# Kernel optimization log

Measured on AMD Instinct MI355X. Metric: run time of the kernel, lower is better.

The kernel has to match this reference:

```python
import jax, jax.numpy as jnp
import numpy as np

N = 100_000   # total nodes across all subgraphs in batch
E = 1_600_000 # edges (avg degree 16)
B = 1_000     # number of subgraphs
D = 128       # in_dim = out_dim
SZ = N // B   # nodes per subgraph


def setup_inputs() -> dict:
    key = jax.random.key(0)
    ks = jax.random.split(key, 8)
    feat = jax.random.normal(ks[0], (N, D), dtype=jnp.float32)
    edge_src = jax.random.randint(ks[1], (E,), 0, N, dtype=jnp.int32)
    edge_dst = jax.random.randint(ks[2], (E,), 0, N, dtype=jnp.int32)
    # pre-normalized edge weights (is_normed=True path)
    edge_w = jax.random.uniform(ks[3], (E,), dtype=jnp.float32)
    s = 1.0 / np.sqrt(D)
    W1 = jax.random.normal(ks[4], (D, D), dtype=jnp.float32) * s
    W2 = jax.random.normal(ks[5], (D, D), dtype=jnp.float32) * s
    Wp = jax.random.normal(ks[6], (D, D), dtype=jnp.float32) * s
    b1 = jnp.zeros((D,), jnp.float32)
    b2 = jnp.zeros((D,), jnp.float32)
    bp = jnp.zeros((D,), jnp.float32)
    # contiguous equal-size subgraphs; target = first node of each subgraph
    seg_ids = jnp.repeat(jnp.arange(B, dtype=jnp.int32), SZ)
    target = jnp.arange(B, dtype=jnp.int32) * SZ
    size_subg = jnp.full((B,), float(SZ), jnp.float32)
    return dict(feat=feat, edge_w=edge_w, W1=W1, b1=b1, W2=W2, b2=b2,
                Wp=Wp, bp=bp, size_subg=size_subg,
                edge_src=edge_src, edge_dst=edge_dst,
                seg_ids=seg_ids, target=target)


def _gcn_layer(x, src, dst, w, W, b):
    # sparse A_hat @ x : gather src features, weight, scatter-add into dst
    msg = x[src] * w[:, None]                       # [E, D]
    agg = jax.ops.segment_sum(msg, dst, num_segments=N)  # [N, D]
    return jax.nn.relu(agg @ W + b)


def reference(feat, edge_w, W1, b1, W2, b2, Wp, bp, size_subg,
              edge_src, edge_dst, seg_ids, target):
    # two stacked GCN layers (self.structure = [structure1, structure2])
    h1 = _gcn_layer(feat, edge_src, edge_dst, edge_w, W1, b1)
    h2 = _gcn_layer(h1, edge_src, edge_dst, edge_w, W2, b2)
    # ResPool: residual-sum over layer outputs, mean pool per subgraph,
    # add target-node embedding (residual), then linear + relu
    h = h1 + h2                                              # [N, D]
    pooled = jax.ops.segment_sum(h, seg_ids, num_segments=B)
    pooled = pooled / size_subg[:, None] + h[target]         # [B, D]
    emb = jax.nn.relu(pooled @ Wp + bp)
    # F.normalize(p=2, dim=1), eps=1e-12
    norm = jnp.sqrt(jnp.sum(emb * emb, axis=1, keepdims=True))
    emb = emb / jnp.maximum(norm, 1e-12)
    return emb  # EnsembleDummy just returns the single branch
```

## Files before the change

### kernel.cpp

```cpp
#include <hip/hip_runtime.h>

#define DD 128
#define CHUNK 4096
#define BSH 8
#define MAXBK 512
#define CAP 6144

typedef _Float16 half8 __attribute__((ext_vector_type(8)));
typedef _Float16 half4v __attribute__((ext_vector_type(4)));
typedef float floatx4 __attribute__((ext_vector_type(4)));
typedef float floatx2 __attribute__((ext_vector_type(2)));

__global__ __launch_bounds__(256) void k_prep(const float* __restrict__ W1,
                                              _Float16* __restrict__ W1t,
                                              const float* __restrict__ W2,
                                              _Float16* __restrict__ W2t) {
    int idx = blockIdx.x * 256 + threadIdx.x;
    const float* W = (idx < DD * DD) ? W1 : W2;
    _Float16* Wt = (idx < DD * DD) ? W1t : W2t;
    int id = idx & (DD * DD - 1);
    int n = id >> 7, k = id & 127;
    Wt[n * DD + k] = (_Float16)W[k * DD + n];
}

__global__ __launch_bounds__(512) void k_p1g1(const int* __restrict__ src,
                                              const int* __restrict__ dst,
                                              const float* __restrict__ w,
                                              int* __restrict__ gcur,
                                              int2* __restrict__ out, int E, int NB,
                                              int p1Blocks,
                                              const float* __restrict__ A,
                                              const _Float16* __restrict__ Wt,
                                              unsigned char* __restrict__ Y, int nrows) {
    if (blockIdx.x < p1Blocks) {
        __shared__ int2 stg[CHUNK];
        __shared__ unsigned short bok[CHUNK];
        __shared__ int lhist[MAXBK];
        __shared__ int loff[MAXBK];
        __shared__ int lbase[MAXBK];
        __shared__ int lcur[MAXBK];
        int tid = threadIdx.x;
        lhist[tid] = 0;
        __syncthreads();

        int beg = blockIdx.x * CHUNK;
        int end = min(beg + CHUNK, E);
        for (int k = beg + tid; k < end; k += 512)
            atomicAdd(&lhist[dst[k] >> BSH], 1);
        __syncthreads();
        if (tid < 64) {
            int base = tid * 8, v[8], s = 0;
            #pragma unroll
            for (int j = 0; j < 8; ++j) { v[j] = lhist[base + j]; s += v[j]; }
            int scn = s;
            #pragma unroll
            for (int off = 1; off < 64; off <<= 1) {
                int t = __shfl_up(scn, off, 64);
                if (tid >= off) scn += t;
            }
            int ex = scn - s;
            #pragma unroll
            for (int j = 0; j < 8; ++j) { loff[base + j] = ex; lcur[base + j] = ex; ex += v[j]; }
        }
        __syncthreads();
        if (tid < NB) {
            int c = lhist[tid];
            if (c) lbase[tid] = tid * CAP + atomicAdd(&gcur[tid], c);
        }
        __syncthreads();
        for (int k = beg + tid; k < end; k += 512) {
            int d = dst[k];
            int b = d >> BSH;
            int p = atomicAdd(&lcur[b], 1);
            stg[p] = make_int2(src[k] | ((d & ((1 << BSH) - 1)) << 17),
                               __float_as_int(w[k]));
            bok[p] = (unsigned short)b;
        }
        __syncthreads();
        int total = end - beg;
        for (int j = tid; j < total; j += 512) {
            int b = bok[j];
            out[lbase[b] + (j - loff[b])] = stg[j];
        }
    } else {
        int gblk = blockIdx.x - p1Blocks;
        int wave = threadIdx.x >> 6;
        int lane = threadIdx.x & 63;
        int row0 = gblk * 256 + wave * 32;
        int m = lane & 15;
        int q = lane >> 4;
        int r0 = min(row0 + m, nrows - 1);
        int r1 = min(row0 + 16 + m, nrows - 1);

        floatx4 acc[2][8];
        #pragma unroll
        for (int t = 0; t < 2; ++t)
            #pragma unroll
            for (int c = 0; c < 8; ++c)
                acc[t][c] = (floatx4){0.f, 0.f, 0.f, 0.f};

        #pragma unroll
        for (int ks = 0; ks < 4; ++ks) {
            int kbase = ks * 32 + q * 8;
            float4 x0 = *reinterpret_cast<const float4*>(A + (size_t)r0 * DD + kbase);
            float4 x1 = *reinterpret_cast<const float4*>(A + (size_t)r0 * DD + kbase + 4);
            float4 y0 = *reinterpret_cast<const float4*>(A + (size_t)r1 * DD + kbase);
            float4 y1 = *reinterpret_cast<const float4*>(A + (size_t)r1 * DD + kbase + 4);
            half8 a0, a1;
            a0[0]=(_Float16)x0.x; a0[1]=(_Float16)x0.y; a0[2]=(_Float16)x0.z; a0[3]=(_Float16)x0.w;
            a0[4]=(_Float16)x1.x; a0[5]=(_Float16)x1.y; a0[6]=(_Float16)x1.z; a0[7]=(_Float16)x1.w;
            a1[0]=(_Float16)y0.x; a1[1]=(_Float16)y0.y; a1[2]=(_Float16)y0.z; a1[3]=(_Float16)y0.w;
            a1[4]=(_Float16)y1.x; a1[5]=(_Float16)y1.y; a1[6]=(_Float16)y1.z; a1[7]=(_Float16)y1.w;
            #pragma unroll
            for (int c = 0; c < 8; ++c) {
                half8 b = *reinterpret_cast<const half8*>(Wt + (size_t)(c * 16 + m) * DD + kbase);
                acc[0][c] = __builtin_amdgcn_mfma_f32_16x16x32_f16(b, a0, acc[0][c], 0, 0, 0);
                acc[1][c] = __builtin_amdgcn_mfma_f32_16x16x32_f16(b, a1, acc[1][c], 0, 0, 0);
            }
        }

        #pragma unroll
        for (int t = 0; t < 2; ++t) {
            int row = row0 + t * 16 + m;
            if (row >= nrows) continue;
            size_t rb = (size_t)row * DD;
            #pragma unroll
            for (int c = 0; c < 8; ++c) {
                int col = c * 16 + q * 4;
                int u = 0;
                u = __builtin_amdgcn_cvt_pk_fp8_f32(acc[t][c][0], acc[t][c][1], u, false);
                u = __builtin_amdgcn_cvt_pk_fp8_f32(acc[t][c][2], acc[t][c][3], u, true);
                *reinterpret_cast<unsigned int*>(&Y[rb + col]) = (unsigned int)u;
            }
        }
    }
}

__global__ __launch_bounds__(512) void k_pass2(const int2* __restrict__ bkt,
                                               const int* __restrict__ gcur,
                                               int2* __restrict__ rows,
                                               int2* __restrict__ edges, int N) {
    __shared__ int lhist[1 << BSH];
    __shared__ int loff[1 << BSH];
    __shared__ int lcur[1 << BSH];
    int tid = threadIdx.x;
    int b = blockIdx.x;
    int base = b * CAP;
    int nrec = gcur[b];
    int d0 = b << BSH;

    if (tid < (1 << BSH)) lhist[tid] = 0;
    __syncthreads();
    for (int i = tid; i < nrec; i += 512)
        atomicAdd(&lhist[(unsigned)bkt[base + i].x >> 17], 1);
    __syncthreads();
    if (tid < 64) {
        int bs = tid * 4, vv[4], s = 0;
        #pragma unroll
        for (int j = 0; j < 4; ++j) { vv[j] = lhist[bs + j]; s += vv[j]; }
        int scn = s;
        #pragma unroll
        for (int off = 1; off < 64; off <<= 1) {
            int t = __shfl_up(scn, off, 64);
            if (tid >= off) scn += t;
        }
        int ex = scn - s;
        #pragma unroll
        for (int j = 0; j < 4; ++j) {
            loff[bs + j] = ex; lcur[bs + j] = ex; ex += vv[j];
        }
    }
    __syncthreads();
    if (tid < (1 << BSH)) {
        int d = d0 + tid;
        if (d < N)
            rows[d] = make_int2(base + loff[tid], base + loff[tid] + lhist[tid]);
    }
    for (int i = tid; i < nrec; i += 512) {
        int2 r = bkt[base + i];
        int dl = (unsigned)r.x >> 17;
        int p = base + atomicAdd(&lcur[dl], 1);
        edges[p] = make_int2(r.x & 0x1FFFF, r.y);
    }
}

__global__ __launch_bounds__(256) void k_gemm_f16A(const _Float16* __restrict__ A,
                                                   const _Float16* __restrict__ Wt,
                                                   unsigned char* __restrict__ Y,
                                                   int nrows) {
    int wave = threadIdx.x >> 6;
    int lane = threadIdx.x & 63;
    int row0 = blockIdx.x * 128 + wave * 32;
    int m = lane & 15;
    int q = lane >> 4;

    floatx4 acc[2][8];
    #pragma unroll
    for (int t = 0; t < 2; ++t)
        #pragma unroll
        for (int c = 0; c < 8; ++c)
            acc[t][c] = (floatx4){0.f, 0.f, 0.f, 0.f};

    #pragma unroll
    for (int ks = 0; ks < 4; ++ks) {
        int kbase = ks * 32 + q * 8;
        half8 a0 = *reinterpret_cast<const half8*>(A + (size_t)(row0 + m) * DD + kbase);
        half8 a1 = *reinterpret_cast<const half8*>(A + (size_t)(row0 + 16 + m) * DD + kbase);
        #pragma unroll
        for (int c = 0; c < 8; ++c) {
            half8 b = *reinterpret_cast<const half8*>(Wt + (size_t)(c * 16 + m) * DD + kbase);
            acc[0][c] = __builtin_amdgcn_mfma_f32_16x16x32_f16(b, a0, acc[0][c], 0, 0, 0);
            acc[1][c] = __builtin_amdgcn_mfma_f32_16x16x32_f16(b, a1, acc[1][c], 0, 0, 0);
        }
    }

    #pragma unroll
    for (int t = 0; t < 2; ++t) {
        int row = row0 + t * 16 + m;
        if (row >= nrows) continue;
        size_t rb = (size_t)row * DD;
        #pragma unroll
        for (int c = 0; c < 8; ++c) {
            int col = c * 16 + q * 4;
            int u = 0;
            u = __builtin_amdgcn_cvt_pk_fp8_f32(acc[t][c][0], acc[t][c][1], u, false);
            u = __builtin_amdgcn_cvt_pk_fp8_f32(acc[t][c][2], acc[t][c][3], u, true);
            *reinterpret_cast<unsigned int*>(&Y[rb + col]) = (unsigned int)u;
        }
    }
}

__global__ __launch_bounds__(256) void k_agg_eplg(const unsigned char* __restrict__ x,
                                                  const int2* __restrict__ rows,
                                                  const int2* __restrict__ edges,
                                                  const float* __restrict__ bias,
                                                  const _Float16* __restrict__ resid,
                                                  _Float16* __restrict__ out, int N) {
    int gwave = (blockIdx.x * blockDim.x + threadIdx.x) >> 6;
    int lane = threadIdx.x & 63;
    int half = lane >> 5;
    int hl = lane & 31;
    int wid = gwave * 2 + half;
    if (wid >= N) return;
    int g = hl >> 3;
    int sl = hl & 7;
    int2 rr = rows[wid];
    int beg = rr.x, end = rr.y;
    float acc[16];
    #pragma unroll
    for (int j = 0; j < 16; ++j) acc[j] = 0.f;

    int i = beg;
    for (; i + 16 <= end; i += 16) {
        int2 e[4];
        #pragma unroll
        for (int u = 0; u < 4; ++u) e[u] = edges[i + u * 4 + g];
        uint4 v[4];
        #pragma unroll
        for (int u = 0; u < 4; ++u)
            v[u] = *reinterpret_cast<const uint4*>(x + (size_t)e[u].x * DD + sl * 16);
        #pragma unroll
        for (int u = 0; u < 4; ++u) {
            float wv = __int_as_float(e[u].y);
            floatx2 f0 = __builtin_amdgcn_cvt_pk_f32_fp8((int)v[u].x, false);
            floatx2 f1 = __builtin_amdgcn_cvt_pk_f32_fp8((int)v[u].x, true);
            floatx2 f2 = __builtin_amdgcn_cvt_pk_f32_fp8((int)v[u].y, false);
            floatx2 f3 = __builtin_amdgcn_cvt_pk_f32_fp8((int)v[u].y, true);
            floatx2 f4 = __builtin_amdgcn_cvt_pk_f32_fp8((int)v[u].z, false);
            floatx2 f5 = __builtin_amdgcn_cvt_pk_f32_fp8((int)v[u].z, true);
            floatx2 f6 = __builtin_amdgcn_cvt_pk_f32_fp8((int)v[u].w, false);
            floatx2 f7 = __builtin_amdgcn_cvt_pk_f32_fp8((int)v[u].w, true);
            acc[0]  = fmaf(f0[0], wv, acc[0]);  acc[1]  = fmaf(f0[1], wv, acc[1]);
            acc[2]  = fmaf(f1[0], wv, acc[2]);  acc[3]  = fmaf(f1[1], wv, acc[3]);
            acc[4]  = fmaf(f2[0], wv, acc[4]);  acc[5]  = fmaf(f2[1], wv, acc[5]);
            acc[6]  = fmaf(f3[0], wv, acc[6]);  acc[7]  = fmaf(f3[1], wv, acc[7]);
            acc[8]  = fmaf(f4[0], wv, acc[8]);  acc[9]  = fmaf(f4[1], wv, acc[9]);
            acc[10] = fmaf(f5[0], wv, acc[10]); acc[11] = fmaf(f5[1], wv, acc[11]);
            acc[12] = fmaf(f6[0], wv, acc[12]); acc[13] = fmaf(f6[1], wv, acc[13]);
            acc[14] = fmaf(f7[0], wv, acc[14]); acc[15] = fmaf(f7[1], wv, acc[15]);
        }
    }
    if (i < end) {
        int2 e[4];
        int ok[4];
        #pragma unroll
        for (int u = 0; u < 4; ++u) {
            int idx = i + u * 4 + g;
            ok[u] = idx < end;
            e[u] = edges[min(idx, end - 1)];
        }
        uint4 v[4];
        #pragma unroll
        for (int u = 0; u < 4; ++u)
            v[u] = *reinterpret_cast<const uint4*>(x + (size_t)e[u].x * DD + sl * 16);
        #pragma unroll
        for (int u = 0; u < 4; ++u) {
            float wv = ok[u] ? __int_as_float(e[u].y) : 0.f;
            floatx2 f0 = __builtin_amdgcn_cvt_pk_f32_fp8((int)v[u].x, false);
            floatx2 f1 = __builtin_amdgcn_cvt_pk_f32_fp8((int)v[u].x, true);
            floatx2 f2 = __builtin_amdgcn_cvt_pk_f32_fp8((int)v[u].y, false);
            floatx2 f3 = __builtin_amdgcn_cvt_pk_f32_fp8((int)v[u].y, true);
            floatx2 f4 = __builtin_amdgcn_cvt_pk_f32_fp8((int)v[u].z, false);
            floatx2 f5 = __builtin_amdgcn_cvt_pk_f32_fp8((int)v[u].z, true);
            floatx2 f6 = __builtin_amdgcn_cvt_pk_f32_fp8((int)v[u].w, false);
            floatx2 f7 = __builtin_amdgcn_cvt_pk_f32_fp8((int)v[u].w, true);
            acc[0]  = fmaf(f0[0], wv, acc[0]);  acc[1]  = fmaf(f0[1], wv, acc[1]);
            acc[2]  = fmaf(f1[0], wv, acc[2]);  acc[3]  = fmaf(f1[1], wv, acc[3]);
            acc[4]  = fmaf(f2[0], wv, acc[4]);  acc[5]  = fmaf(f2[1], wv, acc[5]);
            acc[6]  = fmaf(f3[0], wv, acc[6]);  acc[7]  = fmaf(f3[1], wv, acc[7]);
            acc[8]  = fmaf(f4[0], wv, acc[8]);  acc[9]  = fmaf(f4[1], wv, acc[9]);
            acc[10] = fmaf(f5[0], wv, acc[10]); acc[11] = fmaf(f5[1], wv, acc[11]);
            acc[12] = fmaf(f6[0], wv, acc[12]); acc[13] = fmaf(f6[1], wv, acc[13]);
            acc[14] = fmaf(f7[0], wv, acc[14]); acc[15] = fmaf(f7[1], wv, acc[15]);
        }
    }
    #pragma unroll
    for (int j = 0; j < 16; ++j) {
        acc[j] += __shfl_xor(acc[j], 8, 64);
        acc[j] += __shfl_xor(acc[j], 16, 64);
    }
    if (g == 0) {
        size_t rb = (size_t)wid * DD + sl * 16;
        float bb[16];
        #pragma unroll
        for (int q = 0; q < 4; ++q) {
            float4 b4 = *reinterpret_cast<const float4*>(&bias[sl * 16 + q * 4]);
            bb[q * 4 + 0] = b4.x; bb[q * 4 + 1] = b4.y;
            bb[q * 4 + 2] = b4.z; bb[q * 4 + 3] = b4.w;
        }
        half8 o0, o1;
        if (resid) {
            half8 r0 = *reinterpret_cast<const half8*>(&resid[rb]);
            half8 r1 = *reinterpret_cast<const half8*>(&resid[rb + 8]);
            #pragma unroll
            for (int j = 0; j < 8; ++j) {
                float v = acc[j] + bb[j];
                v = v > 0.f ? v : 0.f;
                o0[j] = (_Float16)(v + (float)r0[j]);
            }
            #pragma unroll
            for (int j = 0; j < 8; ++j) {
                float v = acc[8 + j] + bb[8 + j];
                v = v > 0.f ? v : 0.f;
                o1[j] = (_Float16)(v + (float)r1[j]);
            }
        } else {
            #pragma unroll
            for (int j = 0; j < 8; ++j) {
                float v = acc[j] + bb[j];
                o0[j] = (_Float16)(v > 0.f ? v : 0.f);
            }
            #pragma unroll
            for (int j = 0; j < 8; ++j) {
                float v = acc[8 + j] + bb[8 + j];
                o1[j] = (_Float16)(v > 0.f ? v : 0.f);
            }
        }
        *reinterpret_cast<half8*>(&out[rb]) = o0;
        *reinterpret_cast<half8*>(&out[rb + 8]) = o1;
    }
}

__global__ __launch_bounds__(256) void k_pool_final(const _Float16* __restrict__ h,
                                                    const int* __restrict__ target,
                                                    const float* __restrict__ size_subg,
                                                    const float* __restrict__ Wp,
                                                    const float* __restrict__ bp,
                                                    float* __restrict__ out, int SZ) {
    __shared__ float part[16][DD];
    __shared__ float p[DD];
    __shared__ float wsum[2];
    int b = blockIdx.x;
    int t = threadIdx.x;
    int c = t & 15;
    int r = t >> 4;
    const _Float16* hp = h + (size_t)b * SZ * DD;
    float s[8] = {0.f, 0.f, 0.f, 0.f, 0.f, 0.f, 0.f, 0.f};
    for (int n = r; n < SZ; n += 16) {
        half8 v = *reinterpret_cast<const half8*>(hp + (size_t)n * DD + c * 8);
        #pragma unroll
        for (int j = 0; j < 8; ++j) s[j] += (float)v[j];
    }
    #pragma unroll
    for (int j = 0; j < 8; ++j) part[r][c * 8 + j] = s[j];
    __syncthreads();
    if (t < DD) {
        float sum = 0.f;
        #pragma unroll
        for (int rr = 0; rr < 16; ++rr) sum += part[rr][t];
        int tg = target[b];
        p[t] = sum / size_subg[b] + (float)h[(size_t)tg * DD + t];
    }
    __syncthreads();
    if (t < DD) {
        float acc = 0.f;
        #pragma unroll 4
        for (int k = 0; k < DD; ++k) acc = fmaf(p[k], Wp[k * DD + t], acc);
        float e = acc + bp[t];
        e = e > 0.f ? e : 0.f;
        float sq = e * e;
        #pragma unroll
        for (int off = 32; off > 0; off >>= 1) sq += __shfl_down(sq, off, 64);
        int lane = t & 63, w = t >> 6;
        if (lane == 0) wsum[w] = sq;
        __syncthreads();
        float norm = sqrtf(wsum[0] + wsum[1]);
        float scale = 1.f / fmaxf(norm, 1e-12f);
        out[b * DD + t] = e * scale;
    } else {
        __syncthreads();
    }
}

extern "C" void kernel_launch(void* const* d_in, const int* in_sizes, int n_in,
                              void* d_out, int out_size, void* d_ws, size_t ws_size,
                              hipStream_t stream) {
    const float* feat      = (const float*)d_in[0];
    const float* edge_w    = (const float*)d_in[1];
    const float* W1        = (const float*)d_in[2];
    const float* b1        = (const float*)d_in[3];
    const float* W2        = (const float*)d_in[4];
    const float* b2        = (const float*)d_in[5];
    const float* Wp        = (const float*)d_in[6];
    const float* bp        = (const float*)d_in[7];
    const float* size_subg = (const float*)d_in[8];
    const int*   edge_src  = (const int*)d_in[9];
    const int*   edge_dst  = (const int*)d_in[10];
    const int*   target    = (const int*)d_in[12];

    const int N  = in_sizes[0] / DD;
    const int E  = in_sizes[1];
    const int B  = in_sizes[8];
    const int SZ = N / B;

    const int P  = ((N + 127) / 128) * 128;
    const int NB = (N + (1 << BSH) - 1) >> BSH;

    char* ws = (char*)d_ws;
    size_t off = 0;
    auto alloc = [&](size_t bytes) {
        void* p = ws + off;
        off += (bytes + 255) & ~(size_t)255;
        return p;
    };
    unsigned char* Y = (unsigned char*)alloc((size_t)P * DD);
    _Float16* h1     = (_Float16*)alloc((size_t)P * DD * 2);
    _Float16* H      = (_Float16*)alloc((size_t)P * DD * 2);
    _Float16* W1t    = (_Float16*)alloc((size_t)DD * DD * 2);
    _Float16* W2t    = (_Float16*)alloc((size_t)DD * DD * 2);
    int2*  rows      = (int2*)alloc((size_t)N * 8);
    int*   gcur      = (int*)alloc((size_t)MAXBK * 4);
    int2*  edges_bkt = (int2*)alloc((size_t)NB * CAP * 8);
    int2*  edges     = (int2*)alloc((size_t)NB * CAP * 8);

    hipMemsetAsync(gcur, 0, (size_t)MAXBK * 4, stream);
    k_prep<<<128, 256, 0, stream>>>(W1, W1t, W2, W2t);

    int p1Blocks = (E + CHUNK - 1) / CHUNK;
    int g1Blocks = (N + 255) / 256;
    k_p1g1<<<p1Blocks + g1Blocks, 512, 0, stream>>>(
        edge_src, edge_dst, edge_w, gcur, edges_bkt, E, NB, p1Blocks,
        feat, W1t, Y, N);

    k_pass2<<<NB, 512, 0, stream>>>(edges_bkt, gcur, rows, edges, N);

    int nodePairs  = (N + 1) / 2;
    int aggBlocks  = (nodePairs * 64 + 255) / 256;
    int gemmBlocks = (N + 127) / 128;

    k_agg_eplg<<<aggBlocks, 256, 0, stream>>>(Y, rows, edges, b1, nullptr, h1, N);
    k_gemm_f16A<<<gemmBlocks, 256, 0, stream>>>(h1, W2t, Y, N);
    k_agg_eplg<<<aggBlocks, 256, 0, stream>>>(Y, rows, edges, b2, h1, H, N);
    k_pool_final<<<B, 256, 0, stream>>>(H, target, size_subg, Wp, bp,
                                        (float*)d_out, SZ);
}
```

Before: 305.2 us.

## Replace atomic bucket offsets with per-chunk histogram, scan, and deterministic scatter

Splits the edge bucketing pass into three steps: a histogram kernel fused with the first GEMM, a per-bucket scan over chunk counts, and a scatter pass that reads precomputed offsets. This replaces the global atomicAdd offset reservation and the memset, which makes the bucket layout deterministic and keeps edges in order within each bucket. The cost is two extra kernel launches, a second read of dst, and a histogram array that must round-trip through global memory.

```diff
diff --git a/kernel.cpp b/kernel.cpp
--- a/kernel.cpp
+++ b/kernel.cpp
@@ -4,6 +4,7 @@
 #define CHUNK 4096
 #define BSH 8
 #define MAXBK 512
+#define MAXCH 512
 #define CAP 6144
 
 typedef _Float16 half8 __attribute__((ext_vector_type(8)));
@@ -23,67 +24,25 @@
     Wt[n * DD + k] = (_Float16)W[k * DD + n];
 }
 
-__global__ __launch_bounds__(512) void k_p1g1(const int* __restrict__ src,
-                                              const int* __restrict__ dst,
-                                              const float* __restrict__ w,
-                                              int* __restrict__ gcur,
-                                              int2* __restrict__ out, int E, int NB,
-                                              int p1Blocks,
-                                              const float* __restrict__ A,
-                                              const _Float16* __restrict__ Wt,
-                                              unsigned char* __restrict__ Y, int nrows) {
-    if (blockIdx.x < p1Blocks) {
-        __shared__ int2 stg[CHUNK];
-        __shared__ unsigned short bok[CHUNK];
+__global__ __launch_bounds__(512) void k_histg1(const int* __restrict__ dst,
+                                                int* __restrict__ histT,
+                                                int E, int nChunks,
+                                                const float* __restrict__ A,
+                                                const _Float16* __restrict__ Wt,
+                                                unsigned char* __restrict__ Y, int nrows) {
+    if (blockIdx.x < nChunks) {
         __shared__ int lhist[MAXBK];
-        __shared__ int loff[MAXBK];
-        __shared__ int lbase[MAXBK];
-        __shared__ int lcur[MAXBK];
         int tid = threadIdx.x;
         lhist[tid] = 0;
         __syncthreads();
-
         int beg = blockIdx.x * CHUNK;
         int end = min(beg + CHUNK, E);
         for (int k = beg + tid; k < end; k += 512)
             atomicAdd(&lhist[dst[k] >> BSH], 1);
         __syncthreads();
-        if (tid < 64) {
-            int base = tid * 8, v[8], s = 0;
-            #pragma unroll
-            for (int j = 0; j < 8; ++j) { v[j] = lhist[base + j]; s += v[j]; }
-            int scn = s;
-            #pragma unroll
-            for (int off = 1; off < 64; off <<= 1) {
-                int t = __shfl_up(scn, off, 64);
-                if (tid >= off) scn += t;
-            }
-            int ex = scn - s;
-            #pragma unroll
-            for (int j = 0; j < 8; ++j) { loff[base + j] = ex; lcur[base + j] = ex; ex += v[j]; }
-        }
-        __syncthreads();
-        if (tid < NB) {
-            int c = lhist[tid];
-            if (c) lbase[tid] = tid * CAP + atomicAdd(&gcur[tid], c);
-        }
-        __syncthreads();
-        for (int k = beg + tid; k < end; k += 512) {
-            int d = dst[k];
-            int b = d >> BSH;
-            int p = atomicAdd(&lcur[b], 1);
-            stg[p] = make_int2(src[k] | ((d & ((1 << BSH) - 1)) << 17),
-                               __float_as_int(w[k]));
-            bok[p] = (unsigned short)b;
-        }
-        __syncthreads();
-        int total = end - beg;
-        for (int j = tid; j < total; j += 512) {
-            int b = bok[j];
-            out[lbase[b] + (j - loff[b])] = stg[j];
-        }
+        histT[tid * MAXCH + blockIdx.x] = lhist[tid];
     } else {
-        int gblk = blockIdx.x - p1Blocks;
+        int gblk = blockIdx.x - nChunks;
         int wave = threadIdx.x >> 6;
         int lane = threadIdx.x & 63;
         int row0 = gblk * 256 + wave * 32;
@@ -133,6 +92,85 @@
                 *reinterpret_cast<unsigned int*>(&Y[rb + col]) = (unsigned int)u;
             }
         }
+    }
+}
+
+__global__ __launch_bounds__(512) void k_scan(int* __restrict__ histT,
+                                              int* __restrict__ gcur, int nChunks) {
+    __shared__ int wsum[8];
+    int b = blockIdx.x;
+    int c = threadIdx.x;
+    int v = (c < nChunks) ? histT[b * MAXCH + c] : 0;
+    int lane = c & 63, wave = c >> 6;
+    int inc = v;
+    #pragma unroll
+    for (int off = 1; off < 64; off <<= 1) {
+        int t = __shfl_up(inc, off, 64);
+        if (lane >= off) inc += t;
+    }
+    if (lane == 63) wsum[wave] = inc;
+    __syncthreads();
+    if (c == 0) {
+        int run = 0;
+        #pragma unroll
+        for (int j = 0; j < 8; ++j) { int t = wsum[j]; wsum[j] = run; run += t; }
+    }
+    __syncthreads();
+    int ex = inc - v + wsum[wave];
+    if (c < nChunks) histT[b * MAXCH + c] = ex;
+    if (c == nChunks - 1) gcur[b] = ex + v;
+}
+
+__global__ __launch_bounds__(512) void k_pass1(const int* __restrict__ src,
+                                               const int* __restrict__ dst,
+                                               const float* __restrict__ w,
+                                               const int* __restrict__ histT,
+                                               int2* __restrict__ out, int E, int NB) {
+    __shared__ int2 stg[CHUNK];
+    __shared__ unsigned short bok[CHUNK];
+    __shared__ int lhist[MAXBK];
+    __shared__ int loff[MAXBK];
+    __shared__ int lbase[MAXBK];
+    __shared__ int lcur[MAXBK];
+    int tid = threadIdx.x;
+    lhist[tid] = 0;
+    __syncthreads();
+
+    int beg = blockIdx.x * CHUNK;
+    int end = min(beg + CHUNK, E);
+    for (int k = beg + tid; k < end; k += 512)
+        atomicAdd(&lhist[dst[k] >> BSH], 1);
+    __syncthreads();
+    if (tid < 64) {
+        int base = tid * 8, v[8], s = 0;
+        #pragma unroll
+        for (int j = 0; j < 8; ++j) { v[j] = lhist[base + j]; s += v[j]; }
+        int scn = s;
+        #pragma unroll
+        for (int off = 1; off < 64; off <<= 1) {
+            int t = __shfl_up(scn, off, 64);
+            if (tid >= off) scn += t;
+        }
+        int ex = scn - s;
+        #pragma unroll
+        for (int j = 0; j < 8; ++j) { loff[base + j] = ex; lcur[base + j] = ex; ex += v[j]; }
+    }
+    __syncthreads();
+    if (tid < NB)
+        lbase[tid] = tid * CAP + histT[tid * MAXCH + blockIdx.x];
+    for (int k = beg + tid; k < end; k += 512) {
+        int d = dst[k];
+        int b = d >> BSH;
+        int p = atomicAdd(&lcur[b], 1);
+        stg[p] = make_int2(src[k] | ((d & ((1 << BSH) - 1)) << 17),
+                           __float_as_int(w[k]));
+        bok[p] = (unsigned short)b;
+    }
+    __syncthreads();
+    int total = end - beg;
+    for (int j = tid; j < total; j += 512) {
+        int b = bok[j];
+        out[lbase[b] + (j - loff[b])] = stg[j];
     }
 }
 
@@ -435,6 +473,7 @@
 
     const int P  = ((N + 127) / 128) * 128;
     const int NB = (N + (1 << BSH) - 1) >> BSH;
+    const int nChunks = (E + CHUNK - 1) / CHUNK;
 
     char* ws = (char*)d_ws;
     size_t off = 0;
@@ -450,17 +489,20 @@
     _Float16* W2t    = (_Float16*)alloc((size_t)DD * DD * 2);
     int2*  rows      = (int2*)alloc((size_t)N * 8);
     int*   gcur      = (int*)alloc((size_t)MAXBK * 4);
+    int*   histT     = (int*)alloc((size_t)MAXBK * MAXCH * 4);
     int2*  edges_bkt = (int2*)alloc((size_t)NB * CAP * 8);
     int2*  edges     = (int2*)alloc((size_t)NB * CAP * 8);
 
-    hipMemsetAsync(gcur, 0, (size_t)MAXBK * 4, stream);
     k_prep<<<128, 256, 0, stream>>>(W1, W1t, W2, W2t);
 
-    int p1Blocks = (E + CHUNK - 1) / CHUNK;
     int g1Blocks = (N + 255) / 256;
-    k_p1g1<<<p1Blocks + g1Blocks, 512, 0, stream>>>(
-        edge_src, edge_dst, edge_w, gcur, edges_bkt, E, NB, p1Blocks,
-        feat, W1t, Y, N);
+    k_histg1<<<nChunks + g1Blocks, 512, 0, stream>>>(
+        edge_dst, histT, E, nChunks, feat, W1t, Y, N);
+
+    k_scan<<<NB, 512, 0, stream>>>(histT, gcur, nChunks);
+
+    k_pass1<<<nChunks, 512, 0, stream>>>(edge_src, edge_dst, edge_w, histT,
+                                         edges_bkt, E, NB);
 
     k_pass2<<<NB, 512, 0, stream>>>(edges_bkt, gcur, rows, edges, N);
 
```

Result: no change. 308.9 us (+1.2%).
